# Performance work log

Measured on AMD Instinct MI355X. Metric: run time of the kernel, lower is better.

## Reference

```python
import jax, jax.numpy as jnp
import numpy as np

IN_F = 8192
OUT_F = 8192
R = 16
LORA_ALPHA = 32
BLOCK = 64
SCALING = LORA_ALPHA / R  # 2.0
NUMEL = IN_F * OUT_F


def dequantize_4bit(packed, scales):
    # packed: [numel//2] bytes (stored as int32 in [0,255]); element 2i = low nibble, 2i+1 = high nibble
    low = packed & 0xF
    high = (packed >> 4) & 0xF
    q = jnp.stack([low, high], axis=-1).reshape(-1)          # [numel] ints in [0,15]
    flat = q.astype(jnp.float32) - 8.0                        # signed 4-bit
    flat = (flat.reshape(-1, BLOCK) * scales[:, None]).reshape(-1)  # blockwise scale
    return flat.reshape(OUT_F, IN_F)


def setup_inputs() -> dict:
    key = jax.random.key(0)
    k1, k2, k3, k4, k5 = jax.random.split(key, 5)
    x = jax.random.normal(k1, (1, 64, IN_F), dtype=jnp.float32)
    packed_weights = jax.random.randint(k2, (NUMEL // 2,), 0, 256, dtype=jnp.int32)
    block_scales = jax.random.uniform(k3, (NUMEL // BLOCK,), dtype=jnp.float32) * 0.05
    # kaiming_uniform(a=sqrt(5)) on [R, IN_F] -> bound = 1/sqrt(IN_F)
    bound = 1.0 / np.sqrt(IN_F)
    lora_A = jax.random.uniform(k4, (R, IN_F), minval=-bound, maxval=bound, dtype=jnp.float32)
    # original init is zeros; use small randn for a non-trivial baseline
    lora_B = jax.random.normal(k5, (OUT_F, R), dtype=jnp.float32) * 0.02
    return {"x": x, "packed_weights": packed_weights, "block_scales": block_scales,
            "lora_A": lora_A, "lora_B": lora_B}


def reference(x, packed_weights, block_scales, lora_A, lora_B):
    W = dequantize_4bit(packed_weights, block_scales).astype(x.dtype)  # [OUT_F, IN_F]
    base_out = jnp.einsum('bsi,oi->bso', x, W)                         # no bias (bias_buffer=None)
    lora_out = jnp.einsum('bsr,or->bso', jnp.einsum('bsi,ri->bsr', x, lora_A), lora_B) * SCALING
    return base_out + lora_out
```

## Files before the change

### kernel.cpp

```cpp
#include <hip/hip_runtime.h>
#include <hip/hip_bf16.h>

#define IN_F 8192
#define OUT_F 8192
#define SEQ 64
#define LORA_R 16
#define KH 4096

typedef __attribute__((ext_vector_type(4))) float f32x4;
typedef __attribute__((ext_vector_type(4))) int i32x4;
typedef __attribute__((ext_vector_type(8))) unsigned short u16x8;
typedef __attribute__((ext_vector_type(4))) unsigned short u16x4;
typedef _Float16 f16x2 __attribute__((ext_vector_type(2)));
typedef _Float16 f16x8 __attribute__((ext_vector_type(8)));

__global__ __launch_bounds__(256) void k_prep(
    const float* __restrict__ x, const float* __restrict__ A,
    unsigned short* __restrict__ xb, float* __restrict__ t) {
    __shared__ float part[64];
    const int s = blockIdx.x;
    const int w = threadIdx.x >> 6, lane = threadIdx.x & 63;
    const int kbase = w * 2048;
    const float* xr = x + s * IN_F + kbase;

    f32x4 xv[8];
    #pragma unroll
    for (int j = 0; j < 8; ++j) {
        xv[j] = *(const f32x4*)(xr + j * 256 + lane * 4);
        u16x4 h;
        h[0] = __builtin_bit_cast(unsigned short, (_Float16)xv[j].x);
        h[1] = __builtin_bit_cast(unsigned short, (_Float16)xv[j].y);
        h[2] = __builtin_bit_cast(unsigned short, (_Float16)xv[j].z);
        h[3] = __builtin_bit_cast(unsigned short, (_Float16)xv[j].w);
        *(u16x4*)(xb + s * IN_F + kbase + j * 256 + lane * 4) = h;
    }

    float acc[LORA_R];
    #pragma unroll
    for (int r = 0; r < LORA_R; ++r) acc[r] = 0.f;
    #pragma unroll
    for (int r = 0; r < LORA_R; ++r) {
        const float* ar = A + r * IN_F + kbase;
        #pragma unroll
        for (int j = 0; j < 8; ++j) {
            f32x4 av = *(const f32x4*)(ar + j * 256 + lane * 4);
            acc[r] = fmaf(xv[j].x, av.x, acc[r]);
            acc[r] = fmaf(xv[j].y, av.y, acc[r]);
            acc[r] = fmaf(xv[j].z, av.z, acc[r]);
            acc[r] = fmaf(xv[j].w, av.w, acc[r]);
        }
    }
    #pragma unroll
    for (int r = 0; r < LORA_R; ++r) {
        float v = acc[r];
        #pragma unroll
        for (int off = 32; off; off >>= 1) v += __shfl_down(v, off, 64);
        if (lane == 0) part[w * 16 + r] = v;
    }
    __syncthreads();
    if (threadIdx.x < 16)
        t[s * LORA_R + threadIdx.x] = part[threadIdx.x] + part[16 + threadIdx.x] +
                                      part[32 + threadIdx.x] + part[48 + threadIdx.x];
}

__global__ __launch_bounds__(512, 4) void k_main(
    const int* __restrict__ packed, const float* __restrict__ scales,
    const unsigned short* __restrict__ xb, const float* __restrict__ t,
    const float* __restrict__ B, float* __restrict__ out) {
    __shared__ char lds[60928];
    _Float16* xs = (_Float16*)lds;
    int* wt = (int*)(lds + 34816);
    float* scs = (float*)(lds + 52224);
    float* accs = (float*)lds;

    const int tid = threadIdx.x;
    const int n0 = (blockIdx.x >> 1) * 32;
    const int kh = blockIdx.x & 1;
    const int w = tid >> 6, lane = tid & 63;
    const int nh = w >> 2, wkk = w & 3;
    const int q = lane >> 4, c16 = lane & 15;

    {
        int row = tid >> 4, g = tid & 15;
        f32x4 v = *(const f32x4*)(scales + (n0 + row) * (IN_F / 64) + kh * 64 + g * 4);
        *(f32x4*)(scs + row * 68 + g * 4) = v;
    }

    const int xrow = tid >> 3, xseg = tid & 7;
    const int wrow = tid >> 4, wg = tid & 15;
    const unsigned short* xsrc = xb + xrow * IN_F + kh * KH + xseg * 16;
    const int* wsrc = packed + (long)(n0 + wrow) * (IN_F / 2) + kh * (KH / 2) + wg * 4;

    f32x4 acc[4];
    #pragma unroll
    for (int mt = 0; mt < 4; ++mt) acc[mt] = (f32x4){0.f, 0.f, 0.f, 0.f};

    u16x8 gx0, gx1; i32x4 gw;
    gx0 = *(const u16x8*)(xsrc);
    gx1 = *(const u16x8*)(xsrc + 8);
    gw  = *(const i32x4*)(wsrc);
    *(u16x8*)(xs + xrow * 136 + xseg * 16)     = gx0;
    *(u16x8*)(xs + xrow * 136 + xseg * 16 + 8) = gx1;
    *(i32x4*)(wt + wrow * 68 + wg * 4)         = gw;
    __syncthreads();

    const f16x2 c1032 = {(_Float16)1032.0f, (_Float16)1032.0f};

    for (int kt = 0; kt < 32; ++kt) {
        const int cur = kt & 1;
        if (kt < 31) {
            gx0 = *(const u16x8*)(xsrc + (kt + 1) * 128);
            gx1 = *(const u16x8*)(xsrc + (kt + 1) * 128 + 8);
            gw  = *(const i32x4*)(wsrc + (kt + 1) * 64);
        }
        i32x4 pv = *(const i32x4*)(wt + cur * (32 * 68) + (nh * 16 + c16) * 68 + wkk * 16 + q * 4);
        float scf = scs[(nh * 16 + c16) * 68 + kt * 2 + (wkk >> 1)];
        _Float16 sch = (_Float16)scf;
        f16x2 sc2 = {sch, sch};
        f16x8 bf;
        #pragma unroll
        for (int m = 0; m < 4; ++m) {
            unsigned u = ((((unsigned)pv[m] << 12) | (unsigned)pv[m]) & 0x000F000Fu) | 0x64006400u;
            f16x2 h = __builtin_bit_cast(f16x2, u);
            h = (h - c1032) * sc2;
            bf[2 * m] = h.x;
            bf[2 * m + 1] = h.y;
        }
        const _Float16* xbase = xs + cur * (64 * 136) + wkk * 32 + q * 8;
        #pragma unroll
        for (int mt = 0; mt < 4; ++mt) {
            f16x8 af = *(const f16x8*)(xbase + (mt * 16 + c16) * 136);
            acc[mt] = __builtin_amdgcn_mfma_f32_16x16x32_f16(af, bf, acc[mt], 0, 0, 0);
        }
        __syncthreads();
        if (kt < 31) {
            *(u16x8*)(xs + (1 - cur) * (64 * 136) + xrow * 136 + xseg * 16)     = gx0;
            *(u16x8*)(xs + (1 - cur) * (64 * 136) + xrow * 136 + xseg * 16 + 8) = gx1;
            *(i32x4*)(wt + (1 - cur) * (32 * 68) + wrow * 68 + wg * 4)          = gw;
        }
        __syncthreads();
    }

    float* myacc = accs + w * (64 * 17);
    #pragma unroll
    for (int mt = 0; mt < 4; ++mt)
        #pragma unroll
        for (int r = 0; r < 4; ++r)
            myacc[(mt * 16 + q * 4 + r) * 17 + c16] = acc[mt][r];
    __syncthreads();

    #pragma unroll
    for (int j = 0; j < 4; ++j) {
        int p = tid + j * 512;
        int s = p >> 5, c = p & 31;
        const float* ab = accs + (c >> 4) * 4 * (64 * 17) + s * 17 + (c & 15);
        float v = ab[0] + ab[64 * 17] + ab[2 * 64 * 17] + ab[3 * 64 * 17];
        if (kh == 0) {
            const float* tp = t + s * LORA_R;
            const float* bp = B + (n0 + c) * LORA_R;
            f32x4 t0 = *(const f32x4*)tp,       t1 = *(const f32x4*)(tp + 4);
            f32x4 t2 = *(const f32x4*)(tp + 8), t3 = *(const f32x4*)(tp + 12);
            f32x4 b0 = *(const f32x4*)bp,       b1 = *(const f32x4*)(bp + 4);
            f32x4 b2 = *(const f32x4*)(bp + 8), b3 = *(const f32x4*)(bp + 12);
            float lr = t0.x * b0.x + t0.y * b0.y + t0.z * b0.z + t0.w * b0.w
                     + t1.x * b1.x + t1.y * b1.y + t1.z * b1.z + t1.w * b1.w
                     + t2.x * b2.x + t2.y * b2.y + t2.z * b2.z + t2.w * b2.w
                     + t3.x * b3.x + t3.y * b3.y + t3.z * b3.z + t3.w * b3.w;
            v += 2.0f * lr;
        }
        unsafeAtomicAdd(&out[s * OUT_F + n0 + c], v);
    }
}

extern "C" void kernel_launch(void* const* d_in, const int* in_sizes, int n_in,
                              void* d_out, int out_size, void* d_ws, size_t ws_size,
                              hipStream_t stream) {
    const float* x      = (const float*)d_in[0];
    const int* packed   = (const int*)d_in[1];
    const float* scales = (const float*)d_in[2];
    const float* lora_A = (const float*)d_in[3];
    const float* lora_B = (const float*)d_in[4];
    float* out = (float*)d_out;

    unsigned short* xb = (unsigned short*)d_ws;
    float* t = (float*)((char*)d_ws + (size_t)SEQ * IN_F * 2);

    hipMemsetAsync(out, 0, (size_t)SEQ * OUT_F * sizeof(float), stream);
    k_prep<<<SEQ, 256, 0, stream>>>(x, lora_A, xb, t);
    k_main<<<512, 512, 0, stream>>>(packed, scales, xb, t, lora_B, out);
}
```

Before: 234.0 us.

## Split prep kernel and deepen main loop prefetch to two tiles ahead

The prep kernel is split in two. One wide kernel casts x to fp16, and a second kernel computes the LoRA projection t with 512 threads per row and an LDS reduction. The main GEMM loop is unrolled by two and keeps global loads for two future tiles in flight in registers. This drops one of the two barriers per k-step. The extra kernel launch and higher register pressure could offset the gains.

```diff
diff --git a/kernel.cpp b/kernel.cpp
--- a/kernel.cpp
+++ b/kernel.cpp
@@ -10,57 +10,52 @@
 typedef __attribute__((ext_vector_type(4))) float f32x4;
 typedef __attribute__((ext_vector_type(4))) int i32x4;
 typedef __attribute__((ext_vector_type(8))) unsigned short u16x8;
-typedef __attribute__((ext_vector_type(4))) unsigned short u16x4;
 typedef _Float16 f16x2 __attribute__((ext_vector_type(2)));
 typedef _Float16 f16x8 __attribute__((ext_vector_type(8)));
 
-__global__ __launch_bounds__(256) void k_prep(
-    const float* __restrict__ x, const float* __restrict__ A,
-    unsigned short* __restrict__ xb, float* __restrict__ t) {
-    __shared__ float part[64];
+__global__ __launch_bounds__(256) void k_cast(const float* __restrict__ x,
+                                              unsigned short* __restrict__ xb) {
+    const int i = (blockIdx.x * 256 + threadIdx.x) * 8;
+    f32x4 v0 = *(const f32x4*)(x + i);
+    f32x4 v1 = *(const f32x4*)(x + i + 4);
+    u16x8 h;
+    h[0] = __builtin_bit_cast(unsigned short, (_Float16)v0.x);
+    h[1] = __builtin_bit_cast(unsigned short, (_Float16)v0.y);
+    h[2] = __builtin_bit_cast(unsigned short, (_Float16)v0.z);
+    h[3] = __builtin_bit_cast(unsigned short, (_Float16)v0.w);
+    h[4] = __builtin_bit_cast(unsigned short, (_Float16)v1.x);
+    h[5] = __builtin_bit_cast(unsigned short, (_Float16)v1.y);
+    h[6] = __builtin_bit_cast(unsigned short, (_Float16)v1.z);
+    h[7] = __builtin_bit_cast(unsigned short, (_Float16)v1.w);
+    *(u16x8*)(xb + i) = h;
+}
+
+__global__ __launch_bounds__(512) void k_t(const float* __restrict__ x,
+                                           const float* __restrict__ A,
+                                           float* __restrict__ t) {
+    __shared__ float p[LORA_R][33];
     const int s = blockIdx.x;
-    const int w = threadIdx.x >> 6, lane = threadIdx.x & 63;
-    const int kbase = w * 2048;
-    const float* xr = x + s * IN_F + kbase;
-
-    f32x4 xv[8];
-    #pragma unroll
-    for (int j = 0; j < 8; ++j) {
-        xv[j] = *(const f32x4*)(xr + j * 256 + lane * 4);
-        u16x4 h;
-        h[0] = __builtin_bit_cast(unsigned short, (_Float16)xv[j].x);
-        h[1] = __builtin_bit_cast(unsigned short, (_Float16)xv[j].y);
-        h[2] = __builtin_bit_cast(unsigned short, (_Float16)xv[j].z);
-        h[3] = __builtin_bit_cast(unsigned short, (_Float16)xv[j].w);
-        *(u16x4*)(xb + s * IN_F + kbase + j * 256 + lane * 4) = h;
+    const int r = threadIdx.x & 15, seg = threadIdx.x >> 4;
+    const float* xr = x + s * IN_F + seg * 256;
+    const float* ar = A + r * IN_F + seg * 256;
+    float acc = 0.f;
+    #pragma unroll 8
+    for (int j = 0; j < 64; ++j) {
+        f32x4 xv = *(const f32x4*)(xr + j * 4);
+        f32x4 av = *(const f32x4*)(ar + j * 4);
+        acc = fmaf(xv.x, av.x, acc);
+        acc = fmaf(xv.y, av.y, acc);
+        acc = fmaf(xv.z, av.z, acc);
+        acc = fmaf(xv.w, av.w, acc);
     }
-
-    float acc[LORA_R];
-    #pragma unroll
-    for (int r = 0; r < LORA_R; ++r) acc[r] = 0.f;
-    #pragma unroll
-    for (int r = 0; r < LORA_R; ++r) {
-        const float* ar = A + r * IN_F + kbase;
+    p[r][seg] = acc;
+    __syncthreads();
+    if (threadIdx.x < LORA_R) {
+        float v = 0.f;
         #pragma unroll
-        for (int j = 0; j < 8; ++j) {
-            f32x4 av = *(const f32x4*)(ar + j * 256 + lane * 4);
-            acc[r] = fmaf(xv[j].x, av.x, acc[r]);
-            acc[r] = fmaf(xv[j].y, av.y, acc[r]);
-            acc[r] = fmaf(xv[j].z, av.z, acc[r]);
-            acc[r] = fmaf(xv[j].w, av.w, acc[r]);
-        }
+        for (int g = 0; g < 32; ++g) v += p[threadIdx.x][g];
+        t[s * LORA_R + threadIdx.x] = v;
     }
-    #pragma unroll
-    for (int r = 0; r < LORA_R; ++r) {
-        float v = acc[r];
-        #pragma unroll
-        for (int off = 32; off; off >>= 1) v += __shfl_down(v, off, 64);
-        if (lane == 0) part[w * 16 + r] = v;
-    }
-    __syncthreads();
-    if (threadIdx.x < 16)
-        t[s * LORA_R + threadIdx.x] = part[threadIdx.x] + part[16 + threadIdx.x] +
-                                      part[32 + threadIdx.x] + part[48 + threadIdx.x];
 }
 
 __global__ __launch_bounds__(512, 4) void k_main(
@@ -90,30 +85,17 @@
     const int wrow = tid >> 4, wg = tid & 15;
     const unsigned short* xsrc = xb + xrow * IN_F + kh * KH + xseg * 16;
     const int* wsrc = packed + (long)(n0 + wrow) * (IN_F / 2) + kh * (KH / 2) + wg * 4;
+    _Float16* xdst0 = xs + xrow * 136 + xseg * 16;
+    int* wdst0 = wt + wrow * 68 + wg * 4;
 
     f32x4 acc[4];
     #pragma unroll
     for (int mt = 0; mt < 4; ++mt) acc[mt] = (f32x4){0.f, 0.f, 0.f, 0.f};
 
-    u16x8 gx0, gx1; i32x4 gw;
-    gx0 = *(const u16x8*)(xsrc);
-    gx1 = *(const u16x8*)(xsrc + 8);
-    gw  = *(const i32x4*)(wsrc);
-    *(u16x8*)(xs + xrow * 136 + xseg * 16)     = gx0;
-    *(u16x8*)(xs + xrow * 136 + xseg * 16 + 8) = gx1;
-    *(i32x4*)(wt + wrow * 68 + wg * 4)         = gw;
-    __syncthreads();
-
     const f16x2 c1032 = {(_Float16)1032.0f, (_Float16)1032.0f};
 
-    for (int kt = 0; kt < 32; ++kt) {
-        const int cur = kt & 1;
-        if (kt < 31) {
-            gx0 = *(const u16x8*)(xsrc + (kt + 1) * 128);
-            gx1 = *(const u16x8*)(xsrc + (kt + 1) * 128 + 8);
-            gw  = *(const i32x4*)(wsrc + (kt + 1) * 64);
-        }
-        i32x4 pv = *(const i32x4*)(wt + cur * (32 * 68) + (nh * 16 + c16) * 68 + wkk * 16 + q * 4);
+    auto compute = [&](int buf, int kt) {
+        i32x4 pv = *(const i32x4*)(wt + buf * (32 * 68) + (nh * 16 + c16) * 68 + wkk * 16 + q * 4);
         float scf = scs[(nh * 16 + c16) * 68 + kt * 2 + (wkk >> 1)];
         _Float16 sch = (_Float16)scf;
         f16x2 sc2 = {sch, sch};
@@ -126,20 +108,50 @@
             bf[2 * m] = h.x;
             bf[2 * m + 1] = h.y;
         }
-        const _Float16* xbase = xs + cur * (64 * 136) + wkk * 32 + q * 8;
+        const _Float16* xbase = xs + buf * (64 * 136) + wkk * 32 + q * 8;
         #pragma unroll
         for (int mt = 0; mt < 4; ++mt) {
             f16x8 af = *(const f16x8*)(xbase + (mt * 16 + c16) * 136);
             acc[mt] = __builtin_amdgcn_mfma_f32_16x16x32_f16(af, bf, acc[mt], 0, 0, 0);
         }
+    };
+
+    u16x8 a0 = *(const u16x8*)(xsrc);
+    u16x8 b0 = *(const u16x8*)(xsrc + 8);
+    i32x4 w0 = *(const i32x4*)(wsrc);
+    *(u16x8*)xdst0 = a0;
+    *(u16x8*)(xdst0 + 8) = b0;
+    *(i32x4*)wdst0 = w0;
+    u16x8 a1 = *(const u16x8*)(xsrc + 128);
+    u16x8 b1 = *(const u16x8*)(xsrc + 128 + 8);
+    i32x4 w1 = *(const i32x4*)(wsrc + 64);
+    __syncthreads();
+
+    for (int kt = 0; kt < 32; kt += 2) {
+        if (kt + 2 < 32) {
+            a0 = *(const u16x8*)(xsrc + (kt + 2) * 128);
+            b0 = *(const u16x8*)(xsrc + (kt + 2) * 128 + 8);
+            w0 = *(const i32x4*)(wsrc + (kt + 2) * 64);
+        }
+        compute(0, kt);
+        *(u16x8*)(xs + 64 * 136 + xrow * 136 + xseg * 16) = a1;
+        *(u16x8*)(xs + 64 * 136 + xrow * 136 + xseg * 16 + 8) = b1;
+        *(i32x4*)(wt + 32 * 68 + wrow * 68 + wg * 4) = w1;
         __syncthreads();
-        if (kt < 31) {
-            *(u16x8*)(xs + (1 - cur) * (64 * 136) + xrow * 136 + xseg * 16)     = gx0;
-            *(u16x8*)(xs + (1 - cur) * (64 * 136) + xrow * 136 + xseg * 16 + 8) = gx1;
-            *(i32x4*)(wt + (1 - cur) * (32 * 68) + wrow * 68 + wg * 4)          = gw;
+        if (kt + 3 < 32) {
+            a1 = *(const u16x8*)(xsrc + (kt + 3) * 128);
+            b1 = *(const u16x8*)(xsrc + (kt + 3) * 128 + 8);
+            w1 = *(const i32x4*)(wsrc + (kt + 3) * 64);
         }
-        __syncthreads();
+        compute(1, kt + 1);
+        if (kt + 2 < 32) {
+            *(u16x8*)xdst0 = a0;
+            *(u16x8*)(xdst0 + 8) = b0;
+            *(i32x4*)wdst0 = w0;
+            __syncthreads();
+        }
     }
+    __syncthreads();
 
     float* myacc = accs + w * (64 * 17);
     #pragma unroll
@@ -158,14 +170,9 @@
         if (kh == 0) {
             const float* tp = t + s * LORA_R;
             const float* bp = B + (n0 + c) * LORA_R;
-            f32x4 t0 = *(const f32x4*)tp,       t1 = *(const f32x4*)(tp + 4);
-            f32x4 t2 = *(const f32x4*)(tp + 8), t3 = *(const f32x4*)(tp + 12);
-            f32x4 b0 = *(const f32x4*)bp,       b1 = *(const f32x4*)(bp + 4);
-            f32x4 b2 = *(const f32x4*)(bp + 8), b3 = *(const f32x4*)(bp + 12);
-            float lr = t0.x * b0.x + t0.y * b0.y + t0.z * b0.z + t0.w * b0.w
-                     + t1.x * b1.x + t1.y * b1.y + t1.z * b1.z + t1.w * b1.w
-                     + t2.x * b2.x + t2.y * b2.y + t2.z * b2.z + t2.w * b2.w
-                     + t3.x * b3.x + t3.y * b3.y + t3.z * b3.z + t3.w * b3.w;
+            float lr = 0.f;
+            #pragma unroll
+            for (int r = 0; r < LORA_R; ++r) lr = fmaf(tp[r], bp[r], lr);
             v += 2.0f * lr;
         }
         unsafeAtomicAdd(&out[s * OUT_F + n0 + c], v);
@@ -186,6 +193,7 @@
     float* t = (float*)((char*)d_ws + (size_t)SEQ * IN_F * 2);
 
     hipMemsetAsync(out, 0, (size_t)SEQ * OUT_F * sizeof(float), stream);
-    k_prep<<<SEQ, 256, 0, stream>>>(x, lora_A, xb, t);
+    k_cast<<<SEQ * IN_F / (256 * 8), 256, 0, stream>>>(x, xb);
+    k_t<<<SEQ, 512, 0, stream>>>(x, lora_A, t);
     k_main<<<512, 512, 0, stream>>>(packed, scales, xb, t, lora_B, out);
 }
```

Result: slower. 239.9 us (+2.5%).
